# Performance work log

Hardware: AMD Instinct MI355X
Metric: run time of the kernel (lower is better)

Reference implementation:

```python
import jax, jax.numpy as jnp
import numpy as np

B, L, D = 2, 2048, 1024
H = 16
HD = D // H  # 64
WINDOW = 256


def setup_inputs() -> dict:
    key = jax.random.key(0)
    k1, k2, k3 = jax.random.split(key, 3)
    s = 0.02
    return {
        "x": jax.random.normal(k1, (B, L, D), dtype=jnp.float32),
        "w_qkv": jax.random.normal(k2, (D, 3 * D), dtype=jnp.float32) * s,
        "b_qkv": jnp.zeros((3 * D,), dtype=jnp.float32),
        "w_out": jax.random.normal(k3, (D, D), dtype=jnp.float32) * s,
        "b_out": jnp.zeros((D,), dtype=jnp.float32),
    }


def _window_mask(seq_len, window_size, dtype):
    # row i allows cols in [i - w//2, i + w//2] inclusive (symmetric band)
    half = window_size // 2
    i = jnp.arange(seq_len)[:, None]
    j = jnp.arange(seq_len)[None, :]
    allowed = jnp.abs(i - j) <= half
    return jnp.where(allowed, jnp.zeros((), dtype), jnp.asarray(-jnp.inf, dtype))


def reference(x, w_qkv, b_qkv, w_out, b_out):
    b, l, d = x.shape
    qkv = x @ w_qkv + b_qkv                        # [B, L, 3D]
    qkv = qkv.reshape(b, l, 3, H, HD)
    q = jnp.transpose(qkv[:, :, 0], (0, 2, 1, 3))   # [B, H, L, HD]
    k = jnp.transpose(qkv[:, :, 1], (0, 2, 1, 3))
    v = jnp.transpose(qkv[:, :, 2], (0, 2, 1, 3))
    scale = 1.0 / np.sqrt(HD)
    scores = jnp.einsum("bhqd,bhkd->bhqk", q, k) * scale
    scores = scores + _window_mask(l, WINDOW, scores.dtype)[None, None]
    attn = jax.nn.softmax(scores, axis=-1)          # dropout: eval mode (p applied only in training)
    out = jnp.einsum("bhqk,bhkd->bhqd", attn, v)    # [B, H, L, HD]
    out = jnp.transpose(out, (0, 2, 1, 3)).reshape(b, l, d)
    return out @ w_out + b_out
```

## Files before the change

kernel.cpp:

```cpp
#include <hip/hip_runtime.h>
#include <math.h>

#define B_    2
#define L_    2048
#define D_    1024
#define H_    16
#define HD_   64
#define HALF_ 128
#define TQ    32
#define PST   296

typedef __attribute__((ext_vector_type(8))) short short8;
typedef __attribute__((ext_vector_type(4))) float f32x4;

__device__ __forceinline__ unsigned short f2bf(float x) {
  unsigned int u = __float_as_uint(x);
  u = (u + 0x7fffu + ((u >> 16) & 1u)) >> 16;
  return (unsigned short)u;
}

__device__ __forceinline__ void async_cp16(const unsigned short* g, unsigned short* l) {
  __builtin_amdgcn_global_load_lds(
      (const __attribute__((address_space(1))) unsigned int*)g,
      (__attribute__((address_space(3))) unsigned int*)l, 16, 0, 0);
}

__device__ __forceinline__ void tr_round32(const float* __restrict__ in,
                                           unsigned short* __restrict__ hi,
                                           int N, int K, int n0, int k0,
                                           float (*t)[33], int tid) {
  {
    const int kl = tid >> 3, nl = (tid & 7) * 4;
    const float4 v = *(const float4*)&in[(size_t)(k0 + kl) * N + n0 + nl];
    t[kl][nl + 0] = v.x; t[kl][nl + 1] = v.y;
    t[kl][nl + 2] = v.z; t[kl][nl + 3] = v.w;
  }
  __syncthreads();
  {
    const int no = tid >> 3, ko = (tid & 7) * 4;
    ushort4 h;
    h.x = f2bf(t[ko + 0][no]);
    h.y = f2bf(t[ko + 1][no]);
    h.z = f2bf(t[ko + 2][no]);
    h.w = f2bf(t[ko + 3][no]);
    *(ushort4*)&hi[(size_t)(n0 + no) * K + k0 + ko] = h;
  }
}

__global__ __launch_bounds__(256) void prep(const float* __restrict__ x,
                                            unsigned short* __restrict__ x_hi,
                                            const float* __restrict__ w_qkv,
                                            unsigned short* __restrict__ wqkvT,
                                            const float* __restrict__ w_out,
                                            unsigned short* __restrict__ woutT) {
  __shared__ float t[32][33];
  const int bx = blockIdx.x, tid = threadIdx.x;
  if (bx < 4096) {
    const int i = (bx * 256 + tid) * 4;
    const float4 a = *(const float4*)&x[i];
    ushort4 h;
    h.x = f2bf(a.x); h.y = f2bf(a.y); h.z = f2bf(a.z); h.w = f2bf(a.w);
    *(ushort4*)&x_hi[i] = h;
  } else if (bx < 7168) {
    const int tb = bx - 4096;
    tr_round32(w_qkv, wqkvT, 3 * D_, D_, (tb % 96) * 32, (tb / 96) * 32, t, tid);
  } else {
    const int tb = bx - 7168;
    tr_round32(w_out, woutT, D_, D_, (tb % 32) * 32, (tb / 32) * 32, t, tid);
  }
}

__global__ __launch_bounds__(256) void gemm_qkv(const unsigned short* __restrict__ Ah,
                                                const unsigned short* __restrict__ Bh,
                                                const float* __restrict__ bias,
                                                unsigned short* __restrict__ q_hi,
                                                unsigned short* __restrict__ kT,
                                                unsigned short* __restrict__ vTile,
                                                int N, int K) {
  __shared__ unsigned short sm[2 * 4096];
  const int tid  = threadIdx.x;
  const int wave = tid >> 6, lane = tid & 63;
  const int m0 = blockIdx.y * 128, n0 = blockIdx.x * 128;
  const int wm = (wave >> 1) * 64, wn = (wave & 1) * 64;
  const int quad = lane >> 4, ln16 = lane & 15;

  const unsigned short* src = (wave < 2) ? Ah : Bh;
  const int baserow = (wave < 2) ? m0 : n0;
  const int io = (wave & 1) * 4;
  size_t goff[4];
#pragma unroll
  for (int i = 0; i < 4; ++i) {
    const int inst = io + i;
    const int r = inst * 16 + (lane >> 2);
    const int q = (lane & 3) ^ ((r >> 1) & 3);
    goff[i] = (size_t)(baserow + r) * K + q * 8;
  }
  unsigned short* dst0 = &sm[(wave >> 1) * 4096 + io * 512];

  int offA[4], offB[4];
#pragma unroll
  for (int t = 0; t < 4; ++t) {
    const int r = wm + t * 16 + ln16;
    offA[t] = r * 64 + ((quad ^ ((r >> 1) & 3)) * 16);
    const int rn = wn + t * 16 + ln16;
    offB[t] = rn * 64 + ((quad ^ ((rn >> 1) & 3)) * 16);
  }

  f32x4 acc[4][4] = {};
  const char* smb = (const char*)sm;

  for (int k0 = 0; k0 < K; k0 += 32) {
#pragma unroll
    for (int i = 0; i < 4; ++i)
      async_cp16(src + goff[i] + k0,
                 (unsigned short*)((char*)dst0 + i * 1024));
    __syncthreads();

    short8 ah[4], bh[4];
#pragma unroll
    for (int t = 0; t < 4; ++t) {
      ah[t] = *(const short8*)(smb + offA[t]);
      bh[t] = *(const short8*)(smb + 8192 + offB[t]);
    }
#pragma unroll
    for (int t = 0; t < 4; ++t)
#pragma unroll
      for (int u = 0; u < 4; ++u)
        acc[t][u] = __builtin_amdgcn_mfma_f32_16x16x32_bf16(ah[t], bh[u], acc[t][u], 0, 0, 0);
    __syncthreads();
  }

#pragma unroll
  for (int u = 0; u < 4; ++u) {
    const int col = n0 + wn + u * 16 + ln16;
    const float bv = bias[col];
    const int slot = col >> 10;
    const int hd   = col & 1023;
    const int hh_  = hd >> 6;
    const int dg   = (hd & 63) >> 3, di = hd & 7;
#pragma unroll
    for (int t = 0; t < 4; ++t) {
      const int row0 = m0 + wm + t * 16 + quad * 4;
      if (slot == 0) {
#pragma unroll
        for (int e = 0; e < 4; ++e)
          q_hi[(size_t)(row0 + e) * 1024 + hd] = f2bf(acc[t][u][e] + bv);
      } else if (slot == 1) {
#pragma unroll
        for (int e = 0; e < 4; ++e) {
          const int tok = row0 + e;
          const int bb = tok >> 11, j = tok & 2047;
          const size_t o =
              ((((size_t)bb * 16 + hh_) * 8 + dg) * 2048 + j) * 8 + di;
          kT[o] = f2bf(acc[t][u][e] + bv);
        }
      } else {
        const int bb = row0 >> 11, l0 = row0 & 2047;
        ushort4 vh;
        vh.x = f2bf(acc[t][u][0] + bv);
        vh.y = f2bf(acc[t][u][1] + bv);
        vh.z = f2bf(acc[t][u][2] + bv);
        vh.w = f2bf(acc[t][u][3] + bv);
        const size_t o =
            (((size_t)bb * 256 + (l0 >> 3)) * 1024 + hd) * 8 + (l0 & 7);
        *(ushort4*)&vTile[o] = vh;
      }
    }
  }
}

template <int EPI>
__global__ __launch_bounds__(256) void gemm_n64s(const unsigned short* __restrict__ Ah,
                                                 const unsigned short* __restrict__ Bh,
                                                 const float* __restrict__ bias,
                                                 float* __restrict__ C,
                                                 unsigned short* __restrict__ vTile,
                                                 int N, int K) {
  __shared__ unsigned short sm[6144];
  const int tid  = threadIdx.x;
  const int wave = tid >> 6, lane = tid & 63;
  const int m0 = blockIdx.y * 128, n0 = blockIdx.x * 64;
  const int quad = lane >> 4, ln16 = lane & 15;
  const int wm = wave * 32;

  const unsigned short* sptr[3];
  int dstoff[3];
#pragma unroll
  for (int s = 0; s < 3; ++s) {
    const int g = wave * 3 + s;
    const bool isA = g < 8;
    const unsigned short* base = isA ? Ah : Bh;
    const int r0 = isA ? (m0 + g * 16) : (n0 + (g - 8) * 16);
    const int r = r0 + (lane >> 2);
    const int q = (lane & 3) ^ ((r >> 1) & 3);
    sptr[s] = base + (size_t)r * K + q * 8;
    dstoff[s] = isA ? g * 1024 : 8192 + (g - 8) * 1024;
  }

  int offA[2], offB[4];
#pragma unroll
  for (int t = 0; t < 2; ++t) {
    const int r = wm + t * 16 + ln16;
    offA[t] = r * 64 + ((quad ^ ((r >> 1) & 3)) * 16);
  }
#pragma unroll
  for (int u = 0; u < 4; ++u) {
    const int rn = u * 16 + ln16;
    offB[u] = rn * 64 + ((quad ^ ((rn >> 1) & 3)) * 16);
  }

  f32x4 acc[2][4] = {};
  const char* smb = (const char*)sm;

  for (int k0 = 0; k0 < K; k0 += 32) {
#pragma unroll
    for (int s = 0; s < 3; ++s)
      async_cp16(sptr[s] + k0, (unsigned short*)((char*)sm + dstoff[s]));
    __syncthreads();

    short8 ah[2], bh[4];
#pragma unroll
    for (int t = 0; t < 2; ++t) ah[t] = *(const short8*)(smb + offA[t]);
#pragma unroll
    for (int u = 0; u < 4; ++u) bh[u] = *(const short8*)(smb + 8192 + offB[u]);
#pragma unroll
    for (int t = 0; t < 2; ++t)
#pragma unroll
      for (int u = 0; u < 4; ++u)
        acc[t][u] = __builtin_amdgcn_mfma_f32_16x16x32_bf16(ah[t], bh[u], acc[t][u], 0, 0, 0);
    __syncthreads();
  }

#pragma unroll
  for (int u = 0; u < 4; ++u) {
    const int col = n0 + u * 16 + ln16;
    const float bv = bias[col];
#pragma unroll
    for (int t = 0; t < 2; ++t) {
      const int row0 = m0 + wm + t * 16 + quad * 4;
      if (EPI == 0) {
#pragma unroll
        for (int e = 0; e < 4; ++e)
          C[(size_t)(row0 + e) * N + col] = acc[t][u][e] + bv;
      } else {
        const int bb = row0 >> 11, l0 = row0 & 2047;
        ushort4 vh;
        vh.x = f2bf(acc[t][u][0] + bv);
        vh.y = f2bf(acc[t][u][1] + bv);
        vh.z = f2bf(acc[t][u][2] + bv);
        vh.w = f2bf(acc[t][u][3] + bv);
        const size_t o =
            (((size_t)bb * 256 + (l0 >> 3)) * 1024 + col) * 8 + (l0 & 7);
        *(ushort4*)&vTile[o] = vh;
      }
    }
  }
}

__global__ __launch_bounds__(256, 4) void attn_mfma(
    const unsigned short* __restrict__ q_hi,
    const unsigned short* __restrict__ kT,
    const unsigned short* __restrict__ vTile,
    unsigned short* __restrict__ attn_h) {
  __shared__ unsigned short P[TQ * PST];
  __shared__ float redS[2][32];

  const int b   = blockIdx.z;
  const int h   = blockIdx.y;
  const int i0  = blockIdx.x * TQ;
  const int tid = threadIdx.x;
  const int wave = tid >> 6, lane = tid & 63;
  const int quad = lane >> 4, ln16 = lane & 15;
  const int mt = wave >> 1, np = wave & 1;
  const int jlo = i0 - HALF_;
  const int rbase = mt * 16 + quad * 4;

  float s[4] = {0.f, 0.f, 0.f, 0.f};
  {
    const size_t qbase =
        (size_t)(b * L_ + i0 + mt * 16 + ln16) * 1024 + h * 64 + quad * 8;
    const short8 qh0 = *(const short8*)&q_hi[qbase];
    const short8 qh1 = *(const short8*)&q_hi[qbase + 32];

    const size_t kb0 = (((size_t)b * 16 + h) * 8 + quad) * 2048 * 8;
    const size_t kb1 = (((size_t)b * 16 + h) * 8 + quad + 4) * 2048 * 8;

#pragma unroll
    for (int c = 0; c < 9; ++c) {
      const int nt   = np + 2 * c;
      const int jabs = jlo + nt * 16 + ln16;
      const int jcl  = min(max(jabs, 0), L_ - 1);
      const short8 kh0 = *(const short8*)&kT[kb0 + (size_t)jcl * 8];
      const short8 kh1 = *(const short8*)&kT[kb1 + (size_t)jcl * 8];

      f32x4 a = {};
      a = __builtin_amdgcn_mfma_f32_16x16x32_bf16(qh0, kh0, a, 0, 0, 0);
      a = __builtin_amdgcn_mfma_f32_16x16x32_bf16(qh1, kh1, a, 0, 0, 0);

      const int colj = nt * 16 + ln16;
#pragma unroll
      for (int e = 0; e < 4; ++e) {
        const int iabs = i0 + rbase + e;
        const bool ok = (jabs >= 0) && (jabs < L_) && (abs(iabs - jabs) <= HALF_);
        const float ev = ok ? __expf(a[e] * 0.125f) : 0.f;
        s[e] += ev;
        P[(rbase + e) * PST + colj] = f2bf(ev);
      }
    }
  }
#pragma unroll
  for (int e = 0; e < 4; ++e) {
    s[e] += __shfl_xor(s[e], 1);
    s[e] += __shfl_xor(s[e], 2);
    s[e] += __shfl_xor(s[e], 4);
    s[e] += __shfl_xor(s[e], 8);
  }
  if (ln16 == 0) {
#pragma unroll
    for (int e = 0; e < 4; ++e) redS[np][rbase + e] = s[e];
  }
  __syncthreads();
  float rinv[4];
#pragma unroll
  for (int e = 0; e < 4; ++e) rinv[e] = 1.f / (s[e] + redS[np ^ 1][rbase + e]);

  f32x4 o[2] = {};
  {
    const int dp = np;
    const char* pb = (const char*)P;
#pragma unroll
    for (int c = 0; c < 9; ++c) {
      const short8 pf =
          *(const short8*)(pb + (mt * 16 + ln16) * (PST * 2) + c * 64 + quad * 16);
      int j0 = jlo + c * 32 + quad * 8;
      j0 = min(max(j0, 0), L_ - 8);
      const size_t jgbase = ((size_t)b * 256 + (j0 >> 3)) * 1024;
#pragma unroll
      for (int t = 0; t < 2; ++t) {
        const size_t vb = (jgbase + (h * 64 + dp * 32 + t * 16 + ln16)) * 8;
        const short8 vh = *(const short8*)&vTile[vb];
        o[t] = __builtin_amdgcn_mfma_f32_16x16x32_bf16(pf, vh, o[t], 0, 0, 0);
      }
    }
  }

  __syncthreads();
  float* ob = (float*)P;
  {
    const int dp = np;
#pragma unroll
    for (int t = 0; t < 2; ++t)
#pragma unroll
      for (int e = 0; e < 4; ++e)
        ob[(rbase + e) * 68 + dp * 32 + t * 16 + ln16] = o[t][e] * rinv[e];
  }
  __syncthreads();
  {
    const int rr = tid >> 3, ck = tid & 7;
    const float* rp = ob + rr * 68 + ck * 8;
    const float4 f0 = *(const float4*)&rp[0];
    const float4 f1 = *(const float4*)&rp[4];
    short8 hh;
    hh[0] = (short)f2bf(f0.x); hh[1] = (short)f2bf(f0.y);
    hh[2] = (short)f2bf(f0.z); hh[3] = (short)f2bf(f0.w);
    hh[4] = (short)f2bf(f1.x); hh[5] = (short)f2bf(f1.y);
    hh[6] = (short)f2bf(f1.z); hh[7] = (short)f2bf(f1.w);
    const size_t oo = ((size_t)(b * L_ + i0 + rr)) * 1024 + h * 64 + ck * 8;
    *(short8*)&attn_h[oo] = hh;
  }
}

extern "C" void kernel_launch(void* const* d_in, const int* in_sizes, int n_in,
                              void* d_out, int out_size, void* d_ws, size_t ws_size,
                              hipStream_t stream) {
  const float* x     = (const float*)d_in[0];
  const float* w_qkv = (const float*)d_in[1];
  const float* b_qkv = (const float*)d_in[2];
  const float* w_out = (const float*)d_in[3];
  const float* b_out = (const float*)d_in[4];
  float* out = (float*)d_out;

  const int M = B_ * L_;

  char* ws = (char*)d_ws;
  unsigned short* x_hi    = (unsigned short*)(ws + 0);
  unsigned short* wqkvT   = (unsigned short*)(ws + 16777216);
  unsigned short* woutT   = (unsigned short*)(ws + 23068672);
  unsigned short* q_hi    = (unsigned short*)(ws + 25165824);
  unsigned short* kT      = (unsigned short*)(ws + 33554432);
  unsigned short* vTile   = (unsigned short*)(ws + 41943040);
  unsigned short* attn_hi = (unsigned short*)(ws + 0);

  prep<<<8192, 256, 0, stream>>>(x, x_hi, w_qkv, wqkvT, w_out, woutT);
  {
    dim3 g(3072 / 128, M / 128);
    gemm_qkv<<<g, 256, 0, stream>>>(x_hi, wqkvT, b_qkv, q_hi, kT, vTile,
                                    3072, D_);
  }
  {
    dim3 g(L_ / TQ, H_, B_);
    attn_mfma<<<g, 256, 0, stream>>>(q_hi, kT, vTile, attn_hi);
  }
  {
    dim3 g(D_ / 64, M / 128);
    gemm_n64s<0><<<g, 256, 0, stream>>>(attn_hi, woutT, b_out, out,
                                        nullptr, D_, D_);
  }
}
```

Before: 171.4 us.

## Deepen QKV GEMM K-step, swizzle block order, vectorize epilogue stores

The QKV projection GEMM now loads a 64-wide K slice per iteration, with an 8-way XOR swizzled LDS layout, and issues two MFMA sub-steps per barrier pair, which halves the number of synchronizations. Blocks are remapped with a grouped swizzle for better L2 reuse, and the launch bounds request 3 blocks per CU. Operands in the MFMA are swapped so each lane holds 4 consecutive columns, which allows vectorized bias loads and ushort4 stores for Q and K. The V epilogue is staged through LDS so it can be written as 16-byte tiled chunks. The larger LDS footprint and added register pressure may limit occupancy.

```diff
diff --git a/kernel.cpp b/kernel.cpp
--- a/kernel.cpp
+++ b/kernel.cpp
@@ -70,101 +70,157 @@
   }
 }
 
-__global__ __launch_bounds__(256) void gemm_qkv(const unsigned short* __restrict__ Ah,
-                                                const unsigned short* __restrict__ Bh,
-                                                const float* __restrict__ bias,
-                                                unsigned short* __restrict__ q_hi,
-                                                unsigned short* __restrict__ kT,
-                                                unsigned short* __restrict__ vTile,
-                                                int N, int K) {
-  __shared__ unsigned short sm[2 * 4096];
+__global__ __launch_bounds__(256, 3) void gemm_qkv(
+    const unsigned short* __restrict__ Ah,
+    const unsigned short* __restrict__ Bh,
+    const float* __restrict__ bias,
+    unsigned short* __restrict__ q_hi,
+    unsigned short* __restrict__ kT,
+    unsigned short* __restrict__ vTile,
+    int N, int K) {
+  __shared__ char smraw[33792];
   const int tid  = threadIdx.x;
   const int wave = tid >> 6, lane = tid & 63;
-  const int m0 = blockIdx.y * 128, n0 = blockIdx.x * 128;
+
+  const int lin = blockIdx.y * gridDim.x + blockIdx.x;
+  const int swz = (lin & 7) * 96 + (lin >> 3);
+  const int n0 = (swz % 24) * 128, m0 = (swz / 24) * 128;
+
   const int wm = (wave >> 1) * 64, wn = (wave & 1) * 64;
   const int quad = lane >> 4, ln16 = lane & 15;
 
-  const unsigned short* src = (wave < 2) ? Ah : Bh;
-  const int baserow = (wave < 2) ? m0 : n0;
-  const int io = (wave & 1) * 4;
-  size_t goff[4];
-#pragma unroll
-  for (int i = 0; i < 4; ++i) {
-    const int inst = io + i;
-    const int r = inst * 16 + (lane >> 2);
-    const int q = (lane & 3) ^ ((r >> 1) & 3);
-    goff[i] = (size_t)(baserow + r) * K + q * 8;
-  }
-  unsigned short* dst0 = &sm[(wave >> 1) * 4096 + io * 512];
+  const bool isA = wave < 2;
+  const unsigned short* src = isA ? Ah : Bh;
+  const int baserow = isA ? m0 : n0;
+  const int instbase = (wave & 1) * 8;
+  const int dbase = (isA ? 0 : 16384) + instbase * 1024;
+  size_t goff[8];
+#pragma unroll
+  for (int i = 0; i < 8; ++i) {
+    const int r = (instbase + i) * 8 + (lane >> 3);
+    const int c = (lane & 7) ^ (r & 7);
+    goff[i] = (size_t)(baserow + r) * K + c * 8;
+  }
 
   int offA[4], offB[4];
 #pragma unroll
   for (int t = 0; t < 4; ++t) {
     const int r = wm + t * 16 + ln16;
-    offA[t] = r * 64 + ((quad ^ ((r >> 1) & 3)) * 16);
+    offA[t] = r * 128 + ((quad ^ (r & 7)) * 16);
     const int rn = wn + t * 16 + ln16;
-    offB[t] = rn * 64 + ((quad ^ ((rn >> 1) & 3)) * 16);
+    offB[t] = 16384 + rn * 128 + ((quad ^ (rn & 7)) * 16);
   }
 
   f32x4 acc[4][4] = {};
-  const char* smb = (const char*)sm;
-
-  for (int k0 = 0; k0 < K; k0 += 32) {
-#pragma unroll
-    for (int i = 0; i < 4; ++i)
+  const char* smb = (const char*)smraw;
+
+  for (int k0 = 0; k0 < K; k0 += 64) {
+#pragma unroll
+    for (int i = 0; i < 8; ++i)
       async_cp16(src + goff[i] + k0,
-                 (unsigned short*)((char*)dst0 + i * 1024));
+                 (unsigned short*)(smraw + dbase + i * 1024));
     __syncthreads();
 
-    short8 ah[4], bh[4];
+    {
+      short8 ah[4], bh[4];
+#pragma unroll
+      for (int t = 0; t < 4; ++t) {
+        ah[t] = *(const short8*)(smb + offA[t]);
+        bh[t] = *(const short8*)(smb + offB[t]);
+      }
+#pragma unroll
+      for (int t = 0; t < 4; ++t)
+#pragma unroll
+        for (int u = 0; u < 4; ++u)
+          acc[t][u] = __builtin_amdgcn_mfma_f32_16x16x32_bf16(bh[u], ah[t], acc[t][u], 0, 0, 0);
+    }
+    {
+      short8 ah[4], bh[4];
+#pragma unroll
+      for (int t = 0; t < 4; ++t) {
+        ah[t] = *(const short8*)(smb + (offA[t] ^ 64));
+        bh[t] = *(const short8*)(smb + (offB[t] ^ 64));
+      }
+#pragma unroll
+      for (int t = 0; t < 4; ++t)
+#pragma unroll
+        for (int u = 0; u < 4; ++u)
+          acc[t][u] = __builtin_amdgcn_mfma_f32_16x16x32_bf16(bh[u], ah[t], acc[t][u], 0, 0, 0);
+    }
+    __syncthreads();
+  }
+
+  const int slot = n0 >> 10;
+  const int nbase = n0 & 1023;
+
+  if (slot == 0) {
 #pragma unroll
     for (int t = 0; t < 4; ++t) {
-      ah[t] = *(const short8*)(smb + offA[t]);
-      bh[t] = *(const short8*)(smb + 8192 + offB[t]);
-    }
-#pragma unroll
-    for (int t = 0; t < 4; ++t)
-#pragma unroll
-      for (int u = 0; u < 4; ++u)
-        acc[t][u] = __builtin_amdgcn_mfma_f32_16x16x32_bf16(ah[t], bh[u], acc[t][u], 0, 0, 0);
+      const int m = m0 + wm + t * 16 + ln16;
+#pragma unroll
+      for (int u = 0; u < 4; ++u) {
+        const int nl = wn + u * 16 + quad * 4;
+        const float4 bq = *(const float4*)&bias[n0 + nl];
+        ushort4 h;
+        h.x = f2bf(acc[t][u][0] + bq.x);
+        h.y = f2bf(acc[t][u][1] + bq.y);
+        h.z = f2bf(acc[t][u][2] + bq.z);
+        h.w = f2bf(acc[t][u][3] + bq.w);
+        *(ushort4*)&q_hi[(size_t)m * 1024 + nbase + nl] = h;
+      }
+    }
+  } else if (slot == 1) {
+#pragma unroll
+    for (int t = 0; t < 4; ++t) {
+      const int tok = m0 + wm + t * 16 + ln16;
+      const int bb = tok >> 11, j = tok & 2047;
+#pragma unroll
+      for (int u = 0; u < 4; ++u) {
+        const int nl = wn + u * 16 + quad * 4;
+        const float4 bq = *(const float4*)&bias[n0 + nl];
+        const int hd = nbase + nl;
+        const int hh_ = hd >> 6, dg = (hd & 63) >> 3, di = hd & 7;
+        ushort4 h;
+        h.x = f2bf(acc[t][u][0] + bq.x);
+        h.y = f2bf(acc[t][u][1] + bq.y);
+        h.z = f2bf(acc[t][u][2] + bq.z);
+        h.w = f2bf(acc[t][u][3] + bq.w);
+        const size_t o =
+            ((((size_t)bb * 16 + hh_) * 8 + dg) * 2048 + j) * 8 + di;
+        *(ushort4*)&kT[o] = h;
+      }
+    }
+  } else {
+    unsigned short* lt = (unsigned short*)smraw;
+#pragma unroll
+    for (int t = 0; t < 4; ++t) {
+      const int ml = wm + t * 16 + ln16;
+#pragma unroll
+      for (int u = 0; u < 4; ++u) {
+        const int nl = wn + u * 16 + quad * 4;
+        const float4 bq = *(const float4*)&bias[n0 + nl];
+        ushort4 h;
+        h.x = f2bf(acc[t][u][0] + bq.x);
+        h.y = f2bf(acc[t][u][1] + bq.y);
+        h.z = f2bf(acc[t][u][2] + bq.z);
+        h.w = f2bf(acc[t][u][3] + bq.w);
+        *(ushort4*)&lt[ml * 132 + nl] = h;
+      }
+    }
     __syncthreads();
-  }
-
-#pragma unroll
-  for (int u = 0; u < 4; ++u) {
-    const int col = n0 + wn + u * 16 + ln16;
-    const float bv = bias[col];
-    const int slot = col >> 10;
-    const int hd   = col & 1023;
-    const int hh_  = hd >> 6;
-    const int dg   = (hd & 63) >> 3, di = hd & 7;
-#pragma unroll
-    for (int t = 0; t < 4; ++t) {
-      const int row0 = m0 + wm + t * 16 + quad * 4;
-      if (slot == 0) {
-#pragma unroll
-        for (int e = 0; e < 4; ++e)
-          q_hi[(size_t)(row0 + e) * 1024 + hd] = f2bf(acc[t][u][e] + bv);
-      } else if (slot == 1) {
-#pragma unroll
-        for (int e = 0; e < 4; ++e) {
-          const int tok = row0 + e;
-          const int bb = tok >> 11, j = tok & 2047;
-          const size_t o =
-              ((((size_t)bb * 16 + hh_) * 8 + dg) * 2048 + j) * 8 + di;
-          kT[o] = f2bf(acc[t][u][e] + bv);
-        }
-      } else {
-        const int bb = row0 >> 11, l0 = row0 & 2047;
-        ushort4 vh;
-        vh.x = f2bf(acc[t][u][0] + bv);
-        vh.y = f2bf(acc[t][u][1] + bv);
-        vh.z = f2bf(acc[t][u][2] + bv);
-        vh.w = f2bf(acc[t][u][3] + bv);
-        const size_t o =
-            (((size_t)bb * 256 + (l0 >> 3)) * 1024 + hd) * 8 + (l0 & 7);
-        *(ushort4*)&vTile[o] = vh;
-      }
+    const int jg0 = (m0 & 2047) >> 3;
+    const int bb = m0 >> 11;
+#pragma unroll
+    for (int it = 0; it < 8; ++it) {
+      const int chunk = it * 256 + tid;
+      const int hd = chunk & 127, tokg = chunk >> 7;
+      short8 hh;
+#pragma unroll
+      for (int s = 0; s < 8; ++s)
+        hh[s] = (short)lt[(tokg * 8 + s) * 132 + hd];
+      const size_t o =
+          (((size_t)bb * 256 + jg0 + tokg) * 1024 + nbase + hd) * 8;
+      *(short8*)&vTile[o] = hh;
     }
   }
 }
```

New measurement: 161.7 us. -5.7%, faster.
